# Optimization experiments

Measured on AMD Instinct MI355X. Metric: run time of the kernel, lower is better.

The kernel has to match this reference:

```python
import jax, jax.numpy as jnp
import numpy as np

SIGMA_INIT = 1000.0


def setup_inputs() -> dict:
    key = jax.random.key(0)
    k1, k2, k3 = jax.random.split(key, 3)
    B, M, D, S = 1024, 209, 12288, 2
    input_data = jax.random.normal(k1, (B, D), dtype=jnp.float32)
    center = jax.random.normal(k2, (M, D), dtype=jnp.float32)
    sigma = SIGMA_INIT * jnp.ones((M,), dtype=jnp.float32)
    W = 50.0 * jax.random.normal(k3, (S, M), dtype=jnp.float32)
    b = jnp.zeros((S,), dtype=jnp.float32)
    return {"input_data": input_data, "center": center, "sigma": sigma, "W": W, "b": b}


def reference(input_data, center, sigma, W, b):
    # Euclidean distance ||x_i - c_j|| via GEMM expansion (avoids [B,M,D] diff tensor)
    x2 = jnp.sum(input_data * input_data, axis=1, keepdims=True)        # [B,1]
    c2 = jnp.sum(center * center, axis=1)[None, :]                      # [1,M]
    d2 = x2 + c2 - 2.0 * (input_data @ center.T)                        # [B,M]
    dist = jnp.sqrt(jnp.maximum(d2, 0.0))
    # Note: original divides the (non-squared) norm by sigma^2, then exp(-.)
    radial = jnp.exp(-dist / (sigma * sigma)[None, :])                  # [B,M]
    return radial @ W.T + b                                             # [B,S]
```

## Files before the change

### kernel.cpp

```cpp
#include <hip/hip_runtime.h>
#include <hip/hip_bf16.h>
#include <stdint.h>

#define B_SZ 1024
#define M_SZ 209
#define MPAD 224
#define D_SZ 12288
#define KC   48
#define KCH  (D_SZ / KC)
#define BK   64
#define NIT  (KCH / BK)
#define NB   16
#define BT   64
#define NCT  14
#define SROW 256
#define SLROW (KC * SROW)

#define CBF_OFF  0u
#define XXP_OFF  (MPAD * D_SZ * 2)
#define CC_OFF   (XXP_OFF + B_SZ * KC * 4)
#define SLAB_OFF (CC_OFF + 1024)

typedef __attribute__((ext_vector_type(8))) short short8;
typedef __attribute__((ext_vector_type(4))) float floatx4;

__device__ __forceinline__ uint32_t pk2(float lo, float hi) {
    union { __hip_bfloat162 h; uint32_t u; } cv;
    cv.h = __float22bfloat162_rn(float2{lo, hi});
    return cv.u;
}

__device__ __forceinline__ float bfbits2f(unsigned short u) {
    union { uint32_t u; float f; } cv;
    cv.u = ((uint32_t)u) << 16;
    return cv.f;
}

__device__ __forceinline__ void gload_lds16(const void* g, void* l) {
    __builtin_amdgcn_global_load_lds(
        (const __attribute__((address_space(1))) void*)g,
        (__attribute__((address_space(3))) void*)l, 16, 0, 0);
}

__global__ __launch_bounds__(256) void rbf_prep(
    const float* __restrict__ c, unsigned short* __restrict__ cbf,
    float* __restrict__ cc)
{
    __shared__ float red[4];
    const int j = blockIdx.x, t = threadIdx.x;
    unsigned short* dst = cbf + (size_t)j * D_SZ;
    float s = 0.f;
    if (j < M_SZ) {
        const float* src = c + (size_t)j * D_SZ;
        for (int i = t * 8; i < D_SZ; i += 2048) {
            float4 v0 = *(const float4*)(src + i);
            float4 v1 = *(const float4*)(src + i + 4);
            s += v0.x*v0.x + v0.y*v0.y + v0.z*v0.z + v0.w*v0.w
               + v1.x*v1.x + v1.y*v1.y + v1.z*v1.z + v1.w*v1.w;
            uint4 w = { pk2(v0.x,v0.y), pk2(v0.z,v0.w), pk2(v1.x,v1.y), pk2(v1.z,v1.w) };
            *(uint4*)(dst + i) = w;
        }
    } else {
        uint4 zz = {0u, 0u, 0u, 0u};
        for (int i = t * 8; i < D_SZ; i += 2048) *(uint4*)(dst + i) = zz;
    }
#pragma unroll
    for (int off = 32; off > 0; off >>= 1) s += __shfl_down(s, off);
    if ((t & 63) == 0) red[t >> 6] = s;
    __syncthreads();
    if (t == 0 && j < M_SZ) cc[j] = red[0] + red[1] + red[2] + red[3];
}

__global__ __launch_bounds__(256, 3) void rbf_main(
    const float* __restrict__ x, const unsigned short* __restrict__ cbf,
    __hip_bfloat16* __restrict__ slab, float* __restrict__ xxp)
{
    __shared__ unsigned short sx[BT * BK];
    __shared__ unsigned short sc[MPAD * BK];

    const int t    = threadIdx.x;
    const int k    = blockIdx.x;
    const int b    = blockIdx.y;
    const int wave = t >> 6, lane = t & 63;
    const int quad = lane >> 4, mrow = lane & 15;
    const int m3   = mrow & 7;

    floatx4 acc[NCT];
    const floatx4 z4 = {0.f, 0.f, 0.f, 0.f};
#pragma unroll
    for (int i = 0; i < NCT; ++i) acc[i] = z4;

    const int r  = t >> 2;
    const int c0 = (t & 3) * 2;
    const float* xp = x + (size_t)(b * BT + r) * D_SZ + (size_t)k * KCH + (t & 3) * 16;

    uint4 xw[NIT][2];
    float sxx = 0.f;
#pragma unroll
    for (int it = 0; it < NIT; ++it) {
        float4 v0 = *(const float4*)(xp + it * BK + 0);
        float4 v1 = *(const float4*)(xp + it * BK + 4);
        float4 v2 = *(const float4*)(xp + it * BK + 8);
        float4 v3 = *(const float4*)(xp + it * BK + 12);
        sxx += v0.x*v0.x + v0.y*v0.y + v0.z*v0.z + v0.w*v0.w
             + v1.x*v1.x + v1.y*v1.y + v1.z*v1.z + v1.w*v1.w
             + v2.x*v2.x + v2.y*v2.y + v2.z*v2.z + v2.w*v2.w
             + v3.x*v3.x + v3.y*v3.y + v3.z*v3.z + v3.w*v3.w;
        xw[it][0] = make_uint4(pk2(v0.x,v0.y), pk2(v0.z,v0.w), pk2(v1.x,v1.y), pk2(v1.z,v1.w));
        xw[it][1] = make_uint4(pk2(v2.x,v2.y), pk2(v2.z,v2.w), pk2(v3.x,v3.y), pk2(v3.z,v3.w));
    }

    unsigned short* xw0 = &sx[r * BK + ((c0    ) ^ (r & 7)) * 8];
    unsigned short* xw1 = &sx[r * BK + ((c0 + 1) ^ (r & 7)) * 8];

    const int lr8 = lane >> 3, lc8 = lane & 7;
    const unsigned short* cpb = cbf + (size_t)lr8 * D_SZ + (size_t)k * KCH
                              + (size_t)((lc8 ^ lr8) * 8);

    const unsigned short* ax0 = &sx[(wave * 16 + mrow) * BK + ((quad    ) ^ m3) * 8];
    const unsigned short* ax1 = &sx[(wave * 16 + mrow) * BK + ((quad + 4) ^ m3) * 8];
    const unsigned short* bx0 = &sc[mrow * BK + ((quad    ) ^ m3) * 8];
    const unsigned short* bx1 = &sc[mrow * BK + ((quad + 4) ^ m3) * 8];

    for (int it = 0; it < NIT; ++it) {
#pragma unroll
        for (int j = 0; j < 7; ++j) {
            const int cr = wave * 7 + j;
            gload_lds16(cpb + (size_t)cr * 8 * D_SZ + it * BK, &sc[cr * 512]);
        }
        *(uint4*)xw0 = xw[it][0];
        *(uint4*)xw1 = xw[it][1];
        __syncthreads();

#pragma unroll
        for (int ks = 0; ks < 2; ++ks) {
            short8 a = *(const short8*)(ks ? ax1 : ax0);
            const unsigned short* bb = ks ? bx1 : bx0;
#pragma unroll
            for (int ct = 0; ct < NCT; ++ct) {
                short8 bf = *(const short8*)(bb + ct * 1024);
                acc[ct] = __builtin_amdgcn_mfma_f32_16x16x32_bf16(a, bf, acc[ct], 0, 0, 0);
            }
        }
        __syncthreads();
    }

    __hip_bfloat16* sd = slab + (size_t)k * SROW;
    const int gi0 = b * BT + wave * 16 + quad * 4;
#pragma unroll
    for (int ct = 0; ct < NCT; ++ct) {
        const int gj = ct * 16 + mrow;
#pragma unroll
        for (int rg = 0; rg < 4; ++rg)
            sd[(size_t)(gi0 + rg) * SLROW + gj] = __float2bfloat16(acc[ct][rg]);
    }

    sxx += __shfl_down(sxx, 2);
    sxx += __shfl_down(sxx, 1);
    if ((t & 3) == 0) xxp[(size_t)(b * BT + r) * KC + k] = sxx;
}

__global__ __launch_bounds__(256) void rbf_fin(
    const __hip_bfloat16* __restrict__ slab, const float* __restrict__ xxp,
    const float* __restrict__ cc, const float* __restrict__ sigma,
    const float* __restrict__ W, const float* __restrict__ bias,
    float* __restrict__ out)
{
    __shared__ float jpart[MPAD * 9];
    __shared__ float jtot[MPAD];
    __shared__ float xsh;

    const int t = threadIdx.x;
    const int i = blockIdx.x;

    if (t < 64) {
        float xv = (t < KC) ? xxp[(size_t)i * KC + t] : 0.f;
#pragma unroll
        for (int off = 32; off > 0; off >>= 1) xv += __shfl_down(xv, off);
        if (t == 0) xsh = xv;
    }

    const int o = t % 28, g = t / 28;
    if (t < 252) {
        const unsigned short* sp = (const unsigned short*)slab
                                 + (size_t)i * SLROW + o * 8;
        float s8[8] = {0.f,0.f,0.f,0.f,0.f,0.f,0.f,0.f};
        for (int kk = g; kk < KC; kk += 9) {
            short8 v = *(const short8*)(sp + kk * SROW);
#pragma unroll
            for (int e = 0; e < 8; ++e) s8[e] += bfbits2f((unsigned short)v[e]);
        }
#pragma unroll
        for (int e = 0; e < 8; ++e) jpart[(o * 8 + e) * 9 + g] = s8[e];
    }
    __syncthreads();

    if (t < MPAD) {
        float d = 0.f;
#pragma unroll
        for (int g2 = 0; g2 < 9; ++g2) d += jpart[t * 9 + g2];
        jtot[t] = d;
    }
    __syncthreads();

    if (t < 64) {
        const float xxi = xsh;
        float a0 = 0.f, a1 = 0.f;
        for (int j = t; j < M_SZ; j += 64) {
            float d2 = fmaxf(xxi + cc[j] - 2.f * jtot[j], 0.f);
            float sg = sigma[j];
            float rad = __expf(-sqrtf(d2) / (sg * sg));
            a0 += rad * W[j];
            a1 += rad * W[M_SZ + j];
        }
#pragma unroll
        for (int off = 32; off > 0; off >>= 1) {
            a0 += __shfl_down(a0, off);
            a1 += __shfl_down(a1, off);
        }
        if (t == 0) {
            out[i * 2 + 0] = a0 + bias[0];
            out[i * 2 + 1] = a1 + bias[1];
        }
    }
}

extern "C" void kernel_launch(void* const* d_in, const int* in_sizes, int n_in,
                              void* d_out, int out_size, void* d_ws, size_t ws_size,
                              hipStream_t stream)
{
    const float* x     = (const float*)d_in[0];
    const float* c     = (const float*)d_in[1];
    const float* sigma = (const float*)d_in[2];
    const float* W     = (const float*)d_in[3];
    const float* bias  = (const float*)d_in[4];
    float* out = (float*)d_out;

    char* ws = (char*)d_ws;
    unsigned short*  cbf  = (unsigned short*)(ws + CBF_OFF);
    float*           xxp  = (float*)(ws + XXP_OFF);
    float*           cc   = (float*)(ws + CC_OFF);
    __hip_bfloat16*  slab = (__hip_bfloat16*)(ws + SLAB_OFF);

    rbf_prep<<<MPAD, 256, 0, stream>>>(c, cbf, cc);
    rbf_main<<<dim3(KC, NB), 256, 0, stream>>>(x, cbf, slab, xxp);
    rbf_fin<<<B_SZ, 256, 0, stream>>>(slab, xxp, cc, sigma, W, bias, out);
}
```

Before: 113.6 us.

## Switch split-K GEMM to 32x32x16 MFMA tiles with padded centers and simpler finisher

The main kernel moves from 16x16x32 MFMA with 14 column tiles per wave to 32x32x16 MFMA, where each wave owns a 32-row by 128-column block. Centers are padded to 256 so the tile grid is even, and the slab row is shrunk to 224 entries. The prep kernel is split into two half-row blocks per center, and the finisher now uses one thread per center with a strided column sum plus a cross-wave reduction. The aim is fewer LDS B-reads per FLOP and better MFMA efficiency, at the cost of computing on extra padded columns and strided slab reads in the finisher.

```diff
diff --git a/kernel.cpp b/kernel.cpp
--- a/kernel.cpp
+++ b/kernel.cpp
@@ -4,7 +4,7 @@
 
 #define B_SZ 1024
 #define M_SZ 209
-#define MPAD 224
+#define MPAD 256
 #define D_SZ 12288
 #define KC   48
 #define KCH  (D_SZ / KC)
@@ -12,17 +12,16 @@
 #define NIT  (KCH / BK)
 #define NB   16
 #define BT   64
-#define NCT  14
-#define SROW 256
+#define SROW 224
 #define SLROW (KC * SROW)
 
 #define CBF_OFF  0u
 #define XXP_OFF  (MPAD * D_SZ * 2)
-#define CC_OFF   (XXP_OFF + B_SZ * KC * 4)
-#define SLAB_OFF (CC_OFF + 1024)
-
-typedef __attribute__((ext_vector_type(8))) short short8;
-typedef __attribute__((ext_vector_type(4))) float floatx4;
+#define CCP_OFF  (XXP_OFF + B_SZ * KC * 4)
+#define SLAB_OFF (CCP_OFF + MPAD * 2 * 4)
+
+typedef __attribute__((ext_vector_type(8)))  short short8;
+typedef __attribute__((ext_vector_type(16))) float floatx16;
 
 __device__ __forceinline__ uint32_t pk2(float lo, float hi) {
     union { __hip_bfloat162 h; uint32_t u; } cv;
@@ -44,15 +43,17 @@
 
 __global__ __launch_bounds__(256) void rbf_prep(
     const float* __restrict__ c, unsigned short* __restrict__ cbf,
-    float* __restrict__ cc)
+    float* __restrict__ ccp)
 {
     __shared__ float red[4];
-    const int j = blockIdx.x, t = threadIdx.x;
-    unsigned short* dst = cbf + (size_t)j * D_SZ;
+    const int j = blockIdx.x >> 1, h = blockIdx.x & 1;
+    const int t = threadIdx.x;
+    const int base = h * (D_SZ / 2);
+    unsigned short* dst = cbf + (size_t)j * D_SZ + base;
     float s = 0.f;
     if (j < M_SZ) {
-        const float* src = c + (size_t)j * D_SZ;
-        for (int i = t * 8; i < D_SZ; i += 2048) {
+        const float* src = c + (size_t)j * D_SZ + base;
+        for (int i = t * 8; i < D_SZ / 2; i += 2048) {
             float4 v0 = *(const float4*)(src + i);
             float4 v1 = *(const float4*)(src + i + 4);
             s += v0.x*v0.x + v0.y*v0.y + v0.z*v0.z + v0.w*v0.w
@@ -62,13 +63,13 @@
         }
     } else {
         uint4 zz = {0u, 0u, 0u, 0u};
-        for (int i = t * 8; i < D_SZ; i += 2048) *(uint4*)(dst + i) = zz;
+        for (int i = t * 8; i < D_SZ / 2; i += 2048) *(uint4*)(dst + i) = zz;
     }
 #pragma unroll
     for (int off = 32; off > 0; off >>= 1) s += __shfl_down(s, off);
     if ((t & 63) == 0) red[t >> 6] = s;
     __syncthreads();
-    if (t == 0 && j < M_SZ) cc[j] = red[0] + red[1] + red[2] + red[3];
+    if (t == 0) ccp[j * 2 + h] = red[0] + red[1] + red[2] + red[3];
 }
 
 __global__ __launch_bounds__(256, 3) void rbf_main(
@@ -82,13 +83,15 @@
     const int k    = blockIdx.x;
     const int b    = blockIdx.y;
     const int wave = t >> 6, lane = t & 63;
-    const int quad = lane >> 4, mrow = lane & 15;
-    const int m3   = mrow & 7;
-
-    floatx4 acc[NCT];
-    const floatx4 z4 = {0.f, 0.f, 0.f, 0.f};
-#pragma unroll
-    for (int i = 0; i < NCT; ++i) acc[i] = z4;
+    const int n = lane & 31, h = lane >> 5, e = lane & 7;
+    const int rowtile = wave & 1;
+    const int ctbase  = (wave >> 1) * 4;
+
+    floatx16 acc[4];
+#pragma unroll
+    for (int i = 0; i < 4; ++i)
+#pragma unroll
+        for (int r2 = 0; r2 < 16; ++r2) acc[i][r2] = 0.f;
 
     const int r  = t >> 2;
     const int c0 = (t & 3) * 2;
@@ -109,7 +112,6 @@
         xw[it][0] = make_uint4(pk2(v0.x,v0.y), pk2(v0.z,v0.w), pk2(v1.x,v1.y), pk2(v1.z,v1.w));
         xw[it][1] = make_uint4(pk2(v2.x,v2.y), pk2(v2.z,v2.w), pk2(v3.x,v3.y), pk2(v3.z,v3.w));
     }
-
     unsigned short* xw0 = &sx[r * BK + ((c0    ) ^ (r & 7)) * 8];
     unsigned short* xw1 = &sx[r * BK + ((c0 + 1) ^ (r & 7)) * 8];
 
@@ -117,15 +119,13 @@
     const unsigned short* cpb = cbf + (size_t)lr8 * D_SZ + (size_t)k * KCH
                               + (size_t)((lc8 ^ lr8) * 8);
 
-    const unsigned short* ax0 = &sx[(wave * 16 + mrow) * BK + ((quad    ) ^ m3) * 8];
-    const unsigned short* ax1 = &sx[(wave * 16 + mrow) * BK + ((quad + 4) ^ m3) * 8];
-    const unsigned short* bx0 = &sc[mrow * BK + ((quad    ) ^ m3) * 8];
-    const unsigned short* bx1 = &sc[mrow * BK + ((quad + 4) ^ m3) * 8];
+    const unsigned short* abase = &sx[(rowtile * 32 + n) * BK];
+    const unsigned short* bbase = &sc[n * BK];
 
     for (int it = 0; it < NIT; ++it) {
 #pragma unroll
-        for (int j = 0; j < 7; ++j) {
-            const int cr = wave * 7 + j;
+        for (int jj = 0; jj < 8; ++jj) {
+            const int cr = wave * 8 + jj;
             gload_lds16(cpb + (size_t)cr * 8 * D_SZ + it * BK, &sc[cr * 512]);
         }
         *(uint4*)xw0 = xw[it][0];
@@ -133,26 +133,30 @@
         __syncthreads();
 
 #pragma unroll
-        for (int ks = 0; ks < 2; ++ks) {
-            short8 a = *(const short8*)(ks ? ax1 : ax0);
-            const unsigned short* bb = ks ? bx1 : bx0;
-#pragma unroll
-            for (int ct = 0; ct < NCT; ++ct) {
-                short8 bf = *(const short8*)(bb + ct * 1024);
-                acc[ct] = __builtin_amdgcn_mfma_f32_16x16x32_bf16(a, bf, acc[ct], 0, 0, 0);
+        for (int ks = 0; ks < 4; ++ks) {
+            const int ch = (((2 * ks + h) ^ e)) * 8;
+            short8 a = *(const short8*)(abase + ch);
+#pragma unroll
+            for (int cc2 = 0; cc2 < 4; ++cc2) {
+                short8 bf = *(const short8*)(bbase + (ctbase + cc2) * 32 * BK + ch);
+                acc[cc2] = __builtin_amdgcn_mfma_f32_32x32x16_bf16(a, bf, acc[cc2], 0, 0, 0);
             }
         }
         __syncthreads();
     }
 
     __hip_bfloat16* sd = slab + (size_t)k * SROW;
-    const int gi0 = b * BT + wave * 16 + quad * 4;
-#pragma unroll
-    for (int ct = 0; ct < NCT; ++ct) {
-        const int gj = ct * 16 + mrow;
-#pragma unroll
-        for (int rg = 0; rg < 4; ++rg)
-            sd[(size_t)(gi0 + rg) * SLROW + gj] = __float2bfloat16(acc[ct][rg]);
+    const int gib = b * BT + rowtile * 32 + 4 * h;
+#pragma unroll
+    for (int cc2 = 0; cc2 < 4; ++cc2) {
+        const int gj = (ctbase + cc2) * 32 + n;
+        if (gj < SROW) {
+#pragma unroll
+            for (int reg = 0; reg < 16; ++reg) {
+                const int gi = gib + (reg & 3) + 8 * (reg >> 2);
+                sd[(size_t)gi * SLROW + gj] = __float2bfloat16(acc[cc2][reg]);
+            }
+        }
     }
 
     sxx += __shfl_down(sxx, 2);
@@ -162,16 +166,23 @@
 
 __global__ __launch_bounds__(256) void rbf_fin(
     const __hip_bfloat16* __restrict__ slab, const float* __restrict__ xxp,
-    const float* __restrict__ cc, const float* __restrict__ sigma,
+    const float* __restrict__ ccp, const float* __restrict__ sigma,
     const float* __restrict__ W, const float* __restrict__ bias,
     float* __restrict__ out)
 {
-    __shared__ float jpart[MPAD * 9];
-    __shared__ float jtot[MPAD];
     __shared__ float xsh;
+    __shared__ float red[8];
 
     const int t = threadIdx.x;
     const int i = blockIdx.x;
+    const int wave = t >> 6, lane = t & 63;
+
+    float s = 0.f;
+    if (t < SROW) {
+        const unsigned short* sp = (const unsigned short*)slab + (size_t)i * SLROW + t;
+#pragma unroll 8
+        for (int kk = 0; kk < KC; ++kk) s += bfbits2f(sp[kk * SROW]);
+    }
 
     if (t < 64) {
         float xv = (t < KC) ? xxp[(size_t)i * KC + t] : 0.f;
@@ -179,50 +190,26 @@
         for (int off = 32; off > 0; off >>= 1) xv += __shfl_down(xv, off);
         if (t == 0) xsh = xv;
     }
-
-    const int o = t % 28, g = t / 28;
-    if (t < 252) {
-        const unsigned short* sp = (const unsigned short*)slab
-                                 + (size_t)i * SLROW + o * 8;
-        float s8[8] = {0.f,0.f,0.f,0.f,0.f,0.f,0.f,0.f};
-        for (int kk = g; kk < KC; kk += 9) {
-            short8 v = *(const short8*)(sp + kk * SROW);
-#pragma unroll
-            for (int e = 0; e < 8; ++e) s8[e] += bfbits2f((unsigned short)v[e]);
-        }
-#pragma unroll
-        for (int e = 0; e < 8; ++e) jpart[(o * 8 + e) * 9 + g] = s8[e];
-    }
     __syncthreads();
 
-    if (t < MPAD) {
-        float d = 0.f;
-#pragma unroll
-        for (int g2 = 0; g2 < 9; ++g2) d += jpart[t * 9 + g2];
-        jtot[t] = d;
-    }
+    float a0 = 0.f, a1 = 0.f;
+    if (t < M_SZ) {
+        const float ccj = ccp[t * 2] + ccp[t * 2 + 1];
+        float d2 = fmaxf(xsh + ccj - 2.f * s, 0.f);
+        float sg = sigma[t];
+        float rad = __expf(-sqrtf(d2) / (sg * sg));
+        a0 = rad * W[t];
+        a1 = rad * W[M_SZ + t];
+    }
+#pragma unroll
+    for (int off = 32; off > 0; off >>= 1) {
+        a0 += __shfl_down(a0, off);
+        a1 += __shfl_down(a1, off);
+    }
+    if (lane == 0) { red[wave * 2] = a0; red[wave * 2 + 1] = a1; }
     __syncthreads();
-
-    if (t < 64) {
-        const float xxi = xsh;
-        float a0 = 0.f, a1 = 0.f;
-        for (int j = t; j < M_SZ; j += 64) {
-            float d2 = fmaxf(xxi + cc[j] - 2.f * jtot[j], 0.f);
-            float sg = sigma[j];
-            float rad = __expf(-sqrtf(d2) / (sg * sg));
-            a0 += rad * W[j];
-            a1 += rad * W[M_SZ + j];
-        }
-#pragma unroll
-        for (int off = 32; off > 0; off >>= 1) {
-            a0 += __shfl_down(a0, off);
-            a1 += __shfl_down(a1, off);
-        }
-        if (t == 0) {
-            out[i * 2 + 0] = a0 + bias[0];
-            out[i * 2 + 1] = a1 + bias[1];
-        }
-    }
+    if (t == 0) out[i * 2 + 0] = red[0] + red[2] + red[4] + red[6] + bias[0];
+    if (t == 1) out[i * 2 + 1] = red[1] + red[3] + red[5] + red[7] + bias[1];
 }
 
 extern "C" void kernel_launch(void* const* d_in, const int* in_sizes, int n_in,
@@ -239,10 +226,10 @@
     char* ws = (char*)d_ws;
     unsigned short*  cbf  = (unsigned short*)(ws + CBF_OFF);
     float*           xxp  = (float*)(ws + XXP_OFF);
-    float*           cc   = (float*)(ws + CC_OFF);
+    float*           ccp  = (float*)(ws + CCP_OFF);
     __hip_bfloat16*  slab = (__hip_bfloat16*)(ws + SLAB_OFF);
 
-    rbf_prep<<<MPAD, 256, 0, stream>>>(c, cbf, cc);
+    rbf_prep<<<MPAD * 2, 256, 0, stream>>>(c, cbf, ccp);
     rbf_main<<<dim3(KC, NB), 256, 0, stream>>>(x, cbf, slab, xxp);
-    rbf_fin<<<B_SZ, 256, 0, stream>>>(slab, xxp, cc, sigma, W, bias, out);
-}
+    rbf_fin<<<B_SZ, 256, 0, stream>>>(slab, xxp, ccp, sigma, W, bias, out);
+}
```

Result: slower. 116.1 us (+2.2%).

## Switch distance GEMM to FP8 MFMA with register-resident X fragments

Applied to the files above, without the earlier changes.

Centers and inputs are quantized to FP8 (e4m3) instead of bf16, and the MFMA switches to the 16x16x32 fp8 variant. This halves center bytes and LDS traffic and raises matrix throughput. X fragments are now loaded straight into registers in MFMA layout, which removes the X LDS staging buffer and its stores. The center tile is prefetched before the loop with a new swizzle. The prep kernel is split into two half-row blocks per center that write partial norms. FP8 rounding makes the dot products much less accurate; this is tolerable only because the large sigma makes the output insensitive to distance errors.

```diff
diff --git a/kernel.cpp b/kernel.cpp
--- a/kernel.cpp
+++ b/kernel.cpp
@@ -7,27 +7,27 @@
 #define MPAD 224
 #define D_SZ 12288
 #define KC   48
-#define KCH  (D_SZ / KC)
-#define BK   64
+#define KCH  256
+#define BK   128
 #define NIT  (KCH / BK)
 #define NB   16
 #define BT   64
 #define NCT  14
-#define SROW 256
+#define SROW 224
 #define SLROW (KC * SROW)
 
 #define CBF_OFF  0u
-#define XXP_OFF  (MPAD * D_SZ * 2)
-#define CC_OFF   (XXP_OFF + B_SZ * KC * 4)
-#define SLAB_OFF (CC_OFF + 1024)
+#define XXP_OFF  (MPAD * D_SZ)
+#define CCP_OFF  (XXP_OFF + B_SZ * KC * 4)
+#define SLAB_OFF (CCP_OFF + MPAD * 2 * 4)
 
 typedef __attribute__((ext_vector_type(8))) short short8;
 typedef __attribute__((ext_vector_type(4))) float floatx4;
 
-__device__ __forceinline__ uint32_t pk2(float lo, float hi) {
-    union { __hip_bfloat162 h; uint32_t u; } cv;
-    cv.h = __float22bfloat162_rn(float2{lo, hi});
-    return cv.u;
+__device__ __forceinline__ uint32_t pk8x4(const float4& v) {
+    int d = __builtin_amdgcn_cvt_pk_fp8_f32(v.x, v.y, 0, false);
+    d     = __builtin_amdgcn_cvt_pk_fp8_f32(v.z, v.w, d, true);
+    return (uint32_t)d;
 }
 
 __device__ __forceinline__ float bfbits2f(unsigned short u) {
@@ -43,106 +43,118 @@
 }
 
 __global__ __launch_bounds__(256) void rbf_prep(
-    const float* __restrict__ c, unsigned short* __restrict__ cbf,
-    float* __restrict__ cc)
+    const float* __restrict__ c, uint8_t* __restrict__ cf8,
+    float* __restrict__ ccp)
 {
     __shared__ float red[4];
-    const int j = blockIdx.x, t = threadIdx.x;
-    unsigned short* dst = cbf + (size_t)j * D_SZ;
+    const int j = blockIdx.x >> 1, h = blockIdx.x & 1;
+    const int t = threadIdx.x;
+    const int base = h * (D_SZ / 2);
+    uint8_t* dst = cf8 + (size_t)j * D_SZ + base;
     float s = 0.f;
     if (j < M_SZ) {
-        const float* src = c + (size_t)j * D_SZ;
-        for (int i = t * 8; i < D_SZ; i += 2048) {
+        const float* src = c + (size_t)j * D_SZ + base;
+        for (int i = t * 8; i < D_SZ / 2; i += 2048) {
             float4 v0 = *(const float4*)(src + i);
             float4 v1 = *(const float4*)(src + i + 4);
             s += v0.x*v0.x + v0.y*v0.y + v0.z*v0.z + v0.w*v0.w
                + v1.x*v1.x + v1.y*v1.y + v1.z*v1.z + v1.w*v1.w;
-            uint4 w = { pk2(v0.x,v0.y), pk2(v0.z,v0.w), pk2(v1.x,v1.y), pk2(v1.z,v1.w) };
-            *(uint4*)(dst + i) = w;
+            uint2 w = { pk8x4(v0), pk8x4(v1) };
+            *(uint2*)(dst + i) = w;
         }
     } else {
-        uint4 zz = {0u, 0u, 0u, 0u};
-        for (int i = t * 8; i < D_SZ; i += 2048) *(uint4*)(dst + i) = zz;
+        uint2 zz = {0u, 0u};
+        for (int i = t * 8; i < D_SZ / 2; i += 2048) *(uint2*)(dst + i) = zz;
     }
 #pragma unroll
     for (int off = 32; off > 0; off >>= 1) s += __shfl_down(s, off);
     if ((t & 63) == 0) red[t >> 6] = s;
     __syncthreads();
-    if (t == 0 && j < M_SZ) cc[j] = red[0] + red[1] + red[2] + red[3];
+    if (t == 0) ccp[j * 2 + h] = red[0] + red[1] + red[2] + red[3];
 }
 
 __global__ __launch_bounds__(256, 3) void rbf_main(
-    const float* __restrict__ x, const unsigned short* __restrict__ cbf,
+    const float* __restrict__ x, const uint8_t* __restrict__ cf8,
     __hip_bfloat16* __restrict__ slab, float* __restrict__ xxp)
 {
-    __shared__ unsigned short sx[BT * BK];
-    __shared__ unsigned short sc[MPAD * BK];
+    __shared__ uint8_t sc[MPAD * BK];
 
     const int t    = threadIdx.x;
     const int k    = blockIdx.x;
     const int b    = blockIdx.y;
     const int wave = t >> 6, lane = t & 63;
     const int quad = lane >> 4, mrow = lane & 15;
-    const int m3   = mrow & 7;
+    const int qh = quad >> 1, ql = quad & 1;
+    const int s2 = (mrow >> 1) & 7;
 
     floatx4 acc[NCT];
     const floatx4 z4 = {0.f, 0.f, 0.f, 0.f};
 #pragma unroll
     for (int i = 0; i < NCT; ++i) acc[i] = z4;
 
-    const int r  = t >> 2;
-    const int c0 = (t & 3) * 2;
-    const float* xp = x + (size_t)(b * BT + r) * D_SZ + (size_t)k * KCH + (t & 3) * 16;
-
-    uint4 xw[NIT][2];
+    const int oE = (((lane & 7) ^ (lane >> 4)) & 7) * 16;
+    const int oO = ((((lane & 7) ^ (lane >> 4)) ^ 4) & 7) * 16;
+    const uint8_t* cpbE = cf8 + (size_t)(lane >> 3) * D_SZ + (size_t)k * KCH + oE;
+    const uint8_t* cpbO = cf8 + (size_t)(lane >> 3) * D_SZ + (size_t)k * KCH + oO;
+
+#pragma unroll
+    for (int jj = 0; jj < 7; ++jj) {
+        const int cr = wave * 7 + jj;
+        const uint8_t* p = ((cr & 1) ? cpbO : cpbE) + (size_t)cr * 8 * D_SZ;
+        gload_lds16(p, &sc[cr * 1024]);
+    }
+
+    const float* xr = x + (size_t)(b * BT + wave * 16 + mrow) * D_SZ
+                    + (size_t)k * KCH + quad * 8;
+    long xa[8];
     float sxx = 0.f;
 #pragma unroll
+    for (int half = 0; half < 2; ++half) {
+        float4 fa[4], fb[4];
+#pragma unroll
+        for (int u = 0; u < 4; ++u) {
+            const int ci = half * 4 + u;
+            const int fo = (ci >> 2) * 128 + (ci & 3) * 32;
+            fa[u] = *(const float4*)(xr + fo);
+            fb[u] = *(const float4*)(xr + fo + 4);
+        }
+#pragma unroll
+        for (int u = 0; u < 4; ++u) {
+            sxx += fa[u].x*fa[u].x + fa[u].y*fa[u].y + fa[u].z*fa[u].z + fa[u].w*fa[u].w
+                 + fb[u].x*fb[u].x + fb[u].y*fb[u].y + fb[u].z*fb[u].z + fb[u].w*fb[u].w;
+            const uint32_t lo = pk8x4(fa[u]);
+            const uint32_t hi = pk8x4(fb[u]);
+            xa[half * 4 + u] = (long)(((uint64_t)hi << 32) | lo);
+        }
+    }
+
+    int boff[4];
+#pragma unroll
+    for (int ks = 0; ks < 4; ++ks)
+        boff[ks] = (((ks * 2 + qh) ^ s2) * 16) + ql * 8;
+    const uint8_t* bbase = &sc[mrow * BK];
+
     for (int it = 0; it < NIT; ++it) {
-        float4 v0 = *(const float4*)(xp + it * BK + 0);
-        float4 v1 = *(const float4*)(xp + it * BK + 4);
-        float4 v2 = *(const float4*)(xp + it * BK + 8);
-        float4 v3 = *(const float4*)(xp + it * BK + 12);
-        sxx += v0.x*v0.x + v0.y*v0.y + v0.z*v0.z + v0.w*v0.w
-             + v1.x*v1.x + v1.y*v1.y + v1.z*v1.z + v1.w*v1.w
-             + v2.x*v2.x + v2.y*v2.y + v2.z*v2.z + v2.w*v2.w
-             + v3.x*v3.x + v3.y*v3.y + v3.z*v3.z + v3.w*v3.w;
-        xw[it][0] = make_uint4(pk2(v0.x,v0.y), pk2(v0.z,v0.w), pk2(v1.x,v1.y), pk2(v1.z,v1.w));
-        xw[it][1] = make_uint4(pk2(v2.x,v2.y), pk2(v2.z,v2.w), pk2(v3.x,v3.y), pk2(v3.z,v3.w));
-    }
-
-    unsigned short* xw0 = &sx[r * BK + ((c0    ) ^ (r & 7)) * 8];
-    unsigned short* xw1 = &sx[r * BK + ((c0 + 1) ^ (r & 7)) * 8];
-
-    const int lr8 = lane >> 3, lc8 = lane & 7;
-    const unsigned short* cpb = cbf + (size_t)lr8 * D_SZ + (size_t)k * KCH
-                              + (size_t)((lc8 ^ lr8) * 8);
-
-    const unsigned short* ax0 = &sx[(wave * 16 + mrow) * BK + ((quad    ) ^ m3) * 8];
-    const unsigned short* ax1 = &sx[(wave * 16 + mrow) * BK + ((quad + 4) ^ m3) * 8];
-    const unsigned short* bx0 = &sc[mrow * BK + ((quad    ) ^ m3) * 8];
-    const unsigned short* bx1 = &sc[mrow * BK + ((quad + 4) ^ m3) * 8];
-
-    for (int it = 0; it < NIT; ++it) {
-#pragma unroll
-        for (int j = 0; j < 7; ++j) {
-            const int cr = wave * 7 + j;
-            gload_lds16(cpb + (size_t)cr * 8 * D_SZ + it * BK, &sc[cr * 512]);
-        }
-        *(uint4*)xw0 = xw[it][0];
-        *(uint4*)xw1 = xw[it][1];
         __syncthreads();
-
-#pragma unroll
-        for (int ks = 0; ks < 2; ++ks) {
-            short8 a = *(const short8*)(ks ? ax1 : ax0);
-            const unsigned short* bb = ks ? bx1 : bx0;
+#pragma unroll
+        for (int ks = 0; ks < 4; ++ks) {
+            const long a = xa[it * 4 + ks];
 #pragma unroll
             for (int ct = 0; ct < NCT; ++ct) {
-                short8 bf = *(const short8*)(bb + ct * 1024);
-                acc[ct] = __builtin_amdgcn_mfma_f32_16x16x32_bf16(a, bf, acc[ct], 0, 0, 0);
+                const long bv = *(const long*)(bbase + ct * 16 * BK + boff[ks]);
+                acc[ct] = __builtin_amdgcn_mfma_f32_16x16x32_fp8_fp8(a, bv, acc[ct], 0, 0, 0);
             }
         }
         __syncthreads();
+        if (it + 1 < NIT) {
+#pragma unroll
+            for (int jj = 0; jj < 7; ++jj) {
+                const int cr = wave * 7 + jj;
+                const uint8_t* p = ((cr & 1) ? cpbO : cpbE)
+                                 + (size_t)cr * 8 * D_SZ + (it + 1) * BK;
+                gload_lds16(p, &sc[cr * 1024]);
+            }
+        }
     }
 
     __hip_bfloat16* sd = slab + (size_t)k * SROW;
@@ -155,14 +167,15 @@
             sd[(size_t)(gi0 + rg) * SLROW + gj] = __float2bfloat16(acc[ct][rg]);
     }
 
-    sxx += __shfl_down(sxx, 2);
-    sxx += __shfl_down(sxx, 1);
-    if ((t & 3) == 0) xxp[(size_t)(b * BT + r) * KC + k] = sxx;
+    sxx += __shfl_down(sxx, 32);
+    sxx += __shfl_down(sxx, 16);
+    if (lane < 16)
+        xxp[(size_t)(b * BT + wave * 16 + lane) * KC + k] = sxx;
 }
 
 __global__ __launch_bounds__(256) void rbf_fin(
     const __hip_bfloat16* __restrict__ slab, const float* __restrict__ xxp,
-    const float* __restrict__ cc, const float* __restrict__ sigma,
+    const float* __restrict__ ccp, const float* __restrict__ sigma,
     const float* __restrict__ W, const float* __restrict__ bias,
     float* __restrict__ out)
 {
@@ -207,7 +220,8 @@
         const float xxi = xsh;
         float a0 = 0.f, a1 = 0.f;
         for (int j = t; j < M_SZ; j += 64) {
-            float d2 = fmaxf(xxi + cc[j] - 2.f * jtot[j], 0.f);
+            const float ccj = ccp[j * 2] + ccp[j * 2 + 1];
+            float d2 = fmaxf(xxi + ccj - 2.f * jtot[j], 0.f);
             float sg = sigma[j];
             float rad = __expf(-sqrtf(d2) / (sg * sg));
             a0 += rad * W[j];
@@ -237,12 +251,12 @@
     float* out = (float*)d_out;
 
     char* ws = (char*)d_ws;
-    unsigned short*  cbf  = (unsigned short*)(ws + CBF_OFF);
-    float*           xxp  = (float*)(ws + XXP_OFF);
-    float*           cc   = (float*)(ws + CC_OFF);
-    __hip_bfloat16*  slab = (__hip_bfloat16*)(ws + SLAB_OFF);
-
-    rbf_prep<<<MPAD, 256, 0, stream>>>(c, cbf, cc);
-    rbf_main<<<dim3(KC, NB), 256, 0, stream>>>(x, cbf, slab, xxp);
-    rbf_fin<<<B_SZ, 256, 0, stream>>>(slab, xxp, cc, sigma, W, bias, out);
-}
+    uint8_t*        cf8  = (uint8_t*)(ws + CBF_OFF);
+    float*          xxp  = (float*)(ws + XXP_OFF);
+    float*          ccp  = (float*)(ws + CCP_OFF);
+    __hip_bfloat16* slab = (__hip_bfloat16*)(ws + SLAB_OFF);
+
+    rbf_prep<<<MPAD * 2, 256, 0, stream>>>(c, cf8, ccp);
+    rbf_main<<<dim3(KC, NB), 256, 0, stream>>>(x, cf8, slab, xxp);
+    rbf_fin<<<B_SZ, 256, 0, stream>>>(slab, xxp, ccp, sigma, W, bias, out);
+}
```

After: 111.7 us. Within noise of the previous version (-1.6%).
